# Kernel optimization log

Measured on AMD Instinct MI355X. Metric: run time of the kernel, lower is better.

Reference implementation:

```python
import jax, jax.numpy as jnp
import numpy as np

EPS = 1e-5  # torch BatchNorm default


def setup_inputs() -> dict:
    key = jax.random.key(0)
    ks = jax.random.split(key, 8)
    B, Q, S, C = 4, 256, 128, 256
    feats = [2 * C, 256, 64, 1]  # opt['num_features']
    inp = {
        "support_features": jax.random.normal(ks[0], (B, S, C), dtype=jnp.float32),
        "query_features": jax.random.normal(ks[1], (B, Q, C), dtype=jnp.float32),
    }
    for i in range(3):
        fan_in, fan_out = feats[i], feats[i + 1]
        std = np.sqrt(2.0 / (fan_in + fan_out))  # xavier_normal on conv weight
        inp[f"W{i}"] = jax.random.normal(ks[2 + i], (fan_out, fan_in), dtype=jnp.float32) * std
        inp[f"b{i}"] = jnp.zeros((fan_out,), dtype=jnp.float32)
        inp[f"g{i}"] = jnp.ones((fan_out,), dtype=jnp.float32)   # BN weight
        inp[f"bt{i}"] = jnp.zeros((fan_out,), dtype=jnp.float32)  # BN bias
    return inp


def _bn_relu(x, g, bt):
    # x: [B, N, C]; BatchNorm1d training-mode stats over batch and length dims
    mean = jnp.mean(x, axis=(0, 1))
    var = jnp.mean(jnp.square(x - mean), axis=(0, 1))  # biased var, as torch BN
    return jax.nn.relu((x - mean) * (g * jax.lax.rsqrt(var + EPS)) + bt)


def reference(support_features, query_features,
              W0, b0, g0, bt0, W1, b1, g1, bt1, W2, b2, g2, bt2):
    B, S, C = support_features.shape
    Q = query_features.shape[1]
    # pairwise concat: [B, Q, S, 2C]
    uq = jnp.broadcast_to(query_features[:, :, None, :], (B, Q, S, C))
    us = jnp.broadcast_to(support_features[:, None, :, :], (B, Q, S, C))
    x = jnp.concatenate([uq, us], axis=3).reshape(B, Q * S, 2 * C)
    # 1x1 conv == matmul over channel dim
    x = _bn_relu(jnp.einsum('bnc,oc->bno', x, W0) + b0, g0, bt0)
    x = _bn_relu(jnp.einsum('bnc,oc->bno', x, W1) + b1, g1, bt1)
    x = _bn_relu(jnp.einsum('bnc,oc->bno', x, W2) + b2, g2, bt2)
    # back to [B, C_out, Q, S]
    return jnp.transpose(x, (0, 2, 1)).reshape(B, -1, Q, S)
```

## Files before the change

### kernel.cpp

```cpp
#include <hip/hip_runtime.h>
#include <hip/hip_bf16.h>


typedef __attribute__((ext_vector_type(4))) float f32x4;
typedef __attribute__((ext_vector_type(8))) short s16x8;

#define BN_EPS 1e-5f
#define INV_N  (1.0f/131072.0f)

__device__ __forceinline__ unsigned pk_bf16(float a, float b) {
  float2 t; t.x = a; t.y = b;
  __hip_bfloat162 h = __float22bfloat162_rn(t);
  return *reinterpret_cast<unsigned*>(&h);
}
__device__ __forceinline__ void split2(float a, float b, unsigned& uh, unsigned& ul) {
  uh = pk_bf16(a, b);
  float ha = __uint_as_float(uh << 16);
  float hb = __uint_as_float(uh & 0xFFFF0000u);
  ul = pk_bf16(a - ha, b - hb);
}

union frag_u { s16x8 v; unsigned u[4]; };

struct Args {
  const float *Sf, *Qf, *W0, *b0, *g0, *bt0, *W1, *b1, *g1, *bt1, *W2, *b2, *g2, *bt2;
  float *Aq, *As, *y2, *ws0s, *ws1f, *ws2f, *out;
  ushort *y1f;
};

__global__ __launch_bounds__(64) void k_g0(Args a)
{
  int bi = blockIdx.x, t = threadIdx.x;
  if (bi == 384) {
    for (int i = t; i < 2048; i += 64) a.ws1f[i] = 0.0f;
    if (t < 32) a.ws2f[t] = 0.0f;
    return;
  }
  int l15 = t & 15, quad = t >> 4;
  int chunk = bi >> 2, ntile = bi & 3;
  bool isQ = (chunk < 64);
  const float* X; float* Out; int m0, koff;
  if (isQ) { m0 = chunk * 16; X = a.Qf; Out = a.Aq; koff = 0; }
  else     { m0 = (chunk - 64) * 16; X = a.Sf; Out = a.As; koff = 256; }
  int n0 = ntile * 64;

  f32x4 acc[4] = {};
#pragma unroll
  for (int ko = 0; ko < 256; ko += 32) {
    const float* row = X + (m0 + l15) * 256 + ko + quad * 8;
    f32x4 v0 = *(const f32x4*)(row);
    f32x4 v1 = *(const f32x4*)(row + 4);
    frag_u ah, al;
#pragma unroll
    for (int j = 0; j < 2; j++) {
      split2(v0[2 * j], v0[2 * j + 1], ah.u[j], al.u[j]);
      split2(v1[2 * j], v1[2 * j + 1], ah.u[2 + j], al.u[2 + j]);
    }
#pragma unroll
    for (int nt = 0; nt < 4; nt++) {
      const float* wrow = a.W0 + (n0 + nt * 16 + l15) * 512 + koff + ko + quad * 8;
      f32x4 w0v = *(const f32x4*)(wrow);
      f32x4 w1v = *(const f32x4*)(wrow + 4);
      frag_u bh, bl;
      split2(w0v[0], w0v[1], bh.u[0], bl.u[0]);
      split2(w0v[2], w0v[3], bh.u[1], bl.u[1]);
      split2(w1v[0], w1v[1], bh.u[2], bl.u[2]);
      split2(w1v[2], w1v[3], bh.u[3], bl.u[3]);
      acc[nt] = __builtin_amdgcn_mfma_f32_16x16x32_bf16(ah.v, bh.v, acc[nt], 0, 0, 0);
      acc[nt] = __builtin_amdgcn_mfma_f32_16x16x32_bf16(al.v, bh.v, acc[nt], 0, 0, 0);
      acc[nt] = __builtin_amdgcn_mfma_f32_16x16x32_bf16(ah.v, bl.v, acc[nt], 0, 0, 0);
    }
  }
#pragma unroll
  for (int nt = 0; nt < 4; nt++) {
    int o = n0 + nt * 16 + l15;
    float bias = isQ ? 0.0f : a.b0[o];
    float cs = 0, cs2 = 0;
#pragma unroll
    for (int r = 0; r < 4; r++) {
      float y = acc[nt][r] + bias;
      Out[(m0 + quad * 4 + r) * 256 + o] = y;
      cs += y; cs2 += y * y;
    }
    cs  += __shfl_xor(cs, 16);  cs  += __shfl_xor(cs, 32);
    cs2 += __shfl_xor(cs2, 16); cs2 += __shfl_xor(cs2, 32);
    if (quad == 0) {
      a.ws0s[chunk * 512 + o] = cs;
      a.ws0s[chunk * 512 + 256 + o] = cs2;
    }
  }
}

__device__ __forceinline__ void bn0_finalize(const Args& a, int t, float* sh_a0c0)
{
  int o = t;
  float sumY = 0, cross = 0, SQ2 = 0, SS2 = 0;
#pragma unroll
  for (int b = 0; b < 4; b++) {
    float sq1 = 0, sq2 = 0, ss1 = 0, ss2 = 0;
#pragma unroll
    for (int c = 0; c < 16; c++) {
      sq1 += a.ws0s[(b * 16 + c) * 512 + o];
      sq2 += a.ws0s[(b * 16 + c) * 512 + 256 + o];
    }
#pragma unroll
    for (int c = 0; c < 8; c++) {
      ss1 += a.ws0s[(64 + b * 8 + c) * 512 + o];
      ss2 += a.ws0s[(64 + b * 8 + c) * 512 + 256 + o];
    }
    SQ2 += sq2; SS2 += ss2;
    sumY += 128.0f * sq1 + 256.0f * ss1;
    cross += sq1 * ss1;
  }
  float mean = sumY * INV_N;
  float var = (128.0f * SQ2 + 256.0f * SS2 + 2.0f * cross) * INV_N - mean * mean;
  float aa = a.g0[o] * rsqrtf(var + BN_EPS);
  sh_a0c0[o] = aa;
  sh_a0c0[256 + o] = a.bt0[o] - mean * aa;
}

__global__ __launch_bounds__(256) void k_m1(Args a)
{
  int bi = blockIdx.x, t = threadIdx.x;
  int w = t >> 6, l = t & 63, l15 = l & 15, quad = l >> 4;
  __shared__ ushort w1f[2048 * 8];
  __shared__ float sh_a0c0[512];
  __shared__ float red[2][4][4][16];

#pragma unroll
  for (int i = 0; i < 8; i++) {
    int fr = i * 256 + t;
    int kk = fr >> 8, r = fr & 255, nt = r >> 6, ln = r & 63;
    const float* src = a.W1 + (nt * 16 + (ln & 15)) * 256 + kk * 32 + (ln >> 4) * 8;
    f32x4 v0 = *(const f32x4*)(src);
    f32x4 v1 = *(const f32x4*)(src + 4);
    frag_u z;
    z.u[0] = pk_bf16(v0[0], v0[1]); z.u[1] = pk_bf16(v0[2], v0[3]);
    z.u[2] = pk_bf16(v1[0], v1[1]); z.u[3] = pk_bf16(v1[2], v1[3]);
    *(s16x8*)(w1f + fr * 8) = z.v;
  }
  bn0_finalize(a, t, sh_a0c0);
  __syncthreads();

  int b_ = bi >> 7, rem = bi & 127, qt = rem >> 3, st = rem & 7;
  const float* asrow = a.As + ((b_ << 7) + st * 16 + l15) * 256;
  const float* aqrow[4];
#pragma unroll
  for (int mt = 0; mt < 4; mt++)
    aqrow[mt] = a.Aq + ((b_ << 8) + qt * 16 + w * 4 + mt) * 256;

  f32x4 acc[4][4] = {};
#pragma unroll
  for (int kk = 0; kk < 8; kk++) {
    int obase = kk * 32 + quad * 8;
    f32x4 a0v0 = *(const f32x4*)(sh_a0c0 + obase);
    f32x4 a0v1 = *(const f32x4*)(sh_a0c0 + obase + 4);
    f32x4 c0v0 = *(const f32x4*)(sh_a0c0 + 256 + obase);
    f32x4 c0v1 = *(const f32x4*)(sh_a0c0 + 256 + obase + 4);
    f32x4 as0 = *(const f32x4*)(asrow + obase);
    f32x4 as1 = *(const f32x4*)(asrow + obase + 4);

    s16x8 zh[4];
#pragma unroll
    for (int mt = 0; mt < 4; mt++) {
      f32x4 aq0 = *(const f32x4*)(aqrow[mt] + obase);
      f32x4 aq1 = *(const f32x4*)(aqrow[mt] + obase + 4);
      f32x4 z0 = (aq0 + as0) * a0v0 + c0v0;
      f32x4 z1 = (aq1 + as1) * a0v1 + c0v1;
      frag_u zz;
      zz.u[0] = pk_bf16(fmaxf(z0[0], 0.0f), fmaxf(z0[1], 0.0f));
      zz.u[1] = pk_bf16(fmaxf(z0[2], 0.0f), fmaxf(z0[3], 0.0f));
      zz.u[2] = pk_bf16(fmaxf(z1[0], 0.0f), fmaxf(z1[1], 0.0f));
      zz.u[3] = pk_bf16(fmaxf(z1[2], 0.0f), fmaxf(z1[3], 0.0f));
      zh[mt] = zz.v;
    }
#pragma unroll
    for (int nt = 0; nt < 4; nt++) {
      s16x8 bw = *(const s16x8*)(w1f + ((kk * 4 + nt) * 64 + l) * 8);
#pragma unroll
      for (int mt = 0; mt < 4; mt++)
        acc[mt][nt] = __builtin_amdgcn_mfma_f32_16x16x32_bf16(zh[mt], bw, acc[mt][nt], 0, 0, 0);
    }
  }

  float biasv[4];
#pragma unroll
  for (int nt = 0; nt < 4; nt++) biasv[nt] = a.b1[nt * 16 + l15];
  float s[4] = {0, 0, 0, 0}, s2[4] = {0, 0, 0, 0};
#pragma unroll
  for (int mt = 0; mt < 4; mt++) {
#pragma unroll
    for (int nt = 0; nt < 4; nt++) {
      float y0 = acc[mt][nt][0] + biasv[nt];
      float y1 = acc[mt][nt][1] + biasv[nt];
      float y2v = acc[mt][nt][2] + biasv[nt];
      float y3 = acc[mt][nt][3] + biasv[nt];
      unsigned u01 = pk_bf16(y0, y1), u23 = pk_bf16(y2v, y3);
      uint2 pk; pk.x = u01; pk.y = u23;
      int slot = (bi * 4 + w) * 16 + mt * 4 + nt;
      *(uint2*)(a.y1f + (size_t)(slot * 64 + l) * 4) = pk;
      float f0 = __uint_as_float(u01 << 16), f1 = __uint_as_float(u01 & 0xFFFF0000u);
      float f2 = __uint_as_float(u23 << 16), f3 = __uint_as_float(u23 & 0xFFFF0000u);
      s[nt]  += f0 + f1 + f2 + f3;
      s2[nt] += f0 * f0 + f1 * f1 + f2 * f2 + f3 * f3;
    }
  }
#pragma unroll
  for (int nt = 0; nt < 4; nt++) {
    float v = s[nt], v2 = s2[nt];
    v  += __shfl_xor(v, 16);  v  += __shfl_xor(v, 32);
    v2 += __shfl_xor(v2, 16); v2 += __shfl_xor(v2, 32);
    if (quad == 0) { red[0][w][nt][l15] = v; red[1][w][nt][l15] = v2; }
  }
  __syncthreads();
  if (t < 128) {
    int which = t >> 6, j = t & 63, nt = j >> 4, jl = j & 15;
    float v = red[which][0][nt][jl] + red[which][1][nt][jl] +
              red[which][2][nt][jl] + red[which][3][nt][jl];
    atomicAdd(&a.ws1f[(bi & 15) * 128 + t], v);
  }
}

__global__ __launch_bounds__(256) void k_p2(Args a)
{
  int p = blockIdx.x, t = threadIdx.x;
  int w = t >> 6, l = t & 63, l15 = l & 15, quad = l >> 4;
  __shared__ float sh_tot[128];
  __shared__ float sh_a1c1[128];
  __shared__ float rs[16], rs2[16];

  if (t < 128) {
    float accv = 0;
#pragma unroll
    for (int c = 0; c < 16; c++) accv += a.ws1f[c * 128 + t];
    sh_tot[t] = accv;
  }
  __syncthreads();
  if (t < 64) {
    float mean = sh_tot[t] * INV_N;
    float var = sh_tot[64 + t] * INV_N - mean * mean;
    float aa = a.g1[t] * rsqrtf(var + BN_EPS);
    sh_a1c1[t] = aa;
    sh_a1c1[64 + t] = a.bt1[t] - mean * aa;
  }
  __syncthreads();

  float a1v[4], c1v[4], w2v[4];
#pragma unroll
  for (int nt = 0; nt < 4; nt++) {
    int j = nt * 16 + l15;
    a1v[nt] = sh_a1c1[j]; c1v[nt] = sh_a1c1[64 + j]; w2v[nt] = a.W2[j];
  }
  float b2v = a.b2[0];
  float ls = 0, ls2 = 0;

#pragma unroll
  for (int task = 0; task < 2; task++) {
    int gw = (p * 4 + w) * 2 + task;
    int bi = gw >> 2, w1 = gw & 3;
    int b = bi >> 7, rem = bi & 127, qt = rem >> 3, st = rem & 7;
#pragma unroll
    for (int mt = 0; mt < 4; mt++) {
      float part[4] = {0, 0, 0, 0};
#pragma unroll
      for (int nt = 0; nt < 4; nt++) {
        int slot = (bi * 4 + w1) * 16 + mt * 4 + nt;
        uint2 v = *(const uint2*)(a.y1f + (size_t)(slot * 64 + l) * 4);
        float f0 = __uint_as_float(v.x << 16), f1 = __uint_as_float(v.x & 0xFFFF0000u);
        float f2 = __uint_as_float(v.y << 16), f3 = __uint_as_float(v.y & 0xFFFF0000u);
        part[0] += fmaxf(a1v[nt] * f0 + c1v[nt], 0.0f) * w2v[nt];
        part[1] += fmaxf(a1v[nt] * f1 + c1v[nt], 0.0f) * w2v[nt];
        part[2] += fmaxf(a1v[nt] * f2 + c1v[nt], 0.0f) * w2v[nt];
        part[3] += fmaxf(a1v[nt] * f3 + c1v[nt], 0.0f) * w2v[nt];
      }
#pragma unroll
      for (int r = 0; r < 4; r++) {
        float pv = part[r];
        pv += __shfl_xor(pv, 1); pv += __shfl_xor(pv, 2);
        pv += __shfl_xor(pv, 4); pv += __shfl_xor(pv, 8);
        part[r] = pv + b2v;
      }
      if (l15 == 0) {
        int q = qt * 16 + w1 * 4 + mt;
        int P = ((b * 256 + q) * 128) + st * 16 + quad * 4;
        f32x4 o;
#pragma unroll
        for (int r = 0; r < 4; r++) { o[r] = part[r]; ls += part[r]; ls2 += part[r] * part[r]; }
        *(f32x4*)(a.y2 + P) = o;
      }
    }
  }
  if (l15 == 0) { rs[t >> 4] = ls; rs2[t >> 4] = ls2; }
  __syncthreads();
  if (t == 0) {
    float sv = 0, sv2 = 0;
#pragma unroll
    for (int i = 0; i < 16; i++) { sv += rs[i]; sv2 += rs2[i]; }
    atomicAdd(&a.ws2f[(p & 15) * 2], sv);
    atomicAdd(&a.ws2f[(p & 15) * 2 + 1], sv2);
  }
}

__global__ __launch_bounds__(256) void k_out(Args a)
{
  int t = threadIdx.x;
  float s = 0, s2 = 0;
#pragma unroll
  for (int c = 0; c < 16; c++) { s += a.ws2f[c * 2]; s2 += a.ws2f[c * 2 + 1]; }
  float mean = s * INV_N;
  float var = s2 * INV_N - mean * mean;
  float aa = a.g2[0] * rsqrtf(var + BN_EPS);
  float cc = a.bt2[0] - mean * aa;
  int i = (blockIdx.x * 256 + t) * 4;
  f32x4 v = *(const f32x4*)(a.y2 + i);
  f32x4 o;
#pragma unroll
  for (int r = 0; r < 4; r++) o[r] = fmaxf(aa * v[r] + cc, 0.0f);
  *(f32x4*)(a.out + i) = o;
}

extern "C" void kernel_launch(void* const* d_in, const int* in_sizes, int n_in,
                              void* d_out, int out_size, void* d_ws, size_t ws_size,
                              hipStream_t stream)
{
  float* ws = (float*)d_ws;
  Args a;
  a.Sf  = (const float*)d_in[0];
  a.Qf  = (const float*)d_in[1];
  a.W0  = (const float*)d_in[2];
  a.b0  = (const float*)d_in[3];
  a.g0  = (const float*)d_in[4];
  a.bt0 = (const float*)d_in[5];
  a.W1  = (const float*)d_in[6];
  a.b1  = (const float*)d_in[7];
  a.g1  = (const float*)d_in[8];
  a.bt1 = (const float*)d_in[9];
  a.W2  = (const float*)d_in[10];
  a.b2  = (const float*)d_in[11];
  a.g2  = (const float*)d_in[12];
  a.bt2 = (const float*)d_in[13];

  a.Aq   = ws;
  a.As   = ws + 262144;
  a.y2   = ws + 393216;
  a.ws0s = ws + 524288;
  a.ws1f = ws + 573440;
  a.ws2f = ws + 575488;
  a.y1f  = (ushort*)(ws + 575552);
  a.out  = (float*)d_out;

  k_g0 <<<385, 64, 0, stream>>>(a);
  k_m1 <<<512, 256, 0, stream>>>(a);
  k_p2 <<<256, 256, 0, stream>>>(a);
  k_out<<<128, 256, 0, stream>>>(a);
}
```

Baseline: 130.5 us.

## Fuse final BatchNorm/ReLU into k_p2 via grid-wide atomic barrier

```diff
diff --git a/kernel.cpp b/kernel.cpp
--- a/kernel.cpp
+++ b/kernel.cpp
@@ -24,7 +24,8 @@
 
 struct Args {
   const float *Sf, *Qf, *W0, *b0, *g0, *bt0, *W1, *b1, *g1, *bt1, *W2, *b2, *g2, *bt2;
-  float *Aq, *As, *y2, *ws0s, *ws1f, *ws2f, *out;
+  float *Aq, *As, *ws0s, *ws1f, *ws2f, *out;
+  unsigned *cnt;
   ushort *y1f;
 };
 
@@ -34,6 +35,7 @@
   if (bi == 384) {
     for (int i = t; i < 2048; i += 64) a.ws1f[i] = 0.0f;
     if (t < 32) a.ws2f[t] = 0.0f;
+    if (t == 0) *a.cnt = 0u;
     return;
   }
   int l15 = t & 15, quad = t >> 4;
@@ -228,6 +230,7 @@
   __shared__ float sh_tot[128];
   __shared__ float sh_a1c1[128];
   __shared__ float rs[16], rs2[16];
+  __shared__ float sh_fin[2];
 
   if (t < 128) {
     float accv = 0;
@@ -253,12 +256,12 @@
   }
   float b2v = a.b2[0];
   float ls = 0, ls2 = 0;
+  float keep[2][4][4];
 
 #pragma unroll
   for (int task = 0; task < 2; task++) {
     int gw = (p * 4 + w) * 2 + task;
     int bi = gw >> 2, w1 = gw & 3;
-    int b = bi >> 7, rem = bi & 127, qt = rem >> 3, st = rem & 7;
 #pragma unroll
     for (int mt = 0; mt < 4; mt++) {
       float part[4] = {0, 0, 0, 0};
@@ -278,45 +281,56 @@
         float pv = part[r];
         pv += __shfl_xor(pv, 1); pv += __shfl_xor(pv, 2);
         pv += __shfl_xor(pv, 4); pv += __shfl_xor(pv, 8);
-        part[r] = pv + b2v;
+        float y = pv + b2v;
+        keep[task][mt][r] = y;
+        if (l15 == 0) { ls += y; ls2 += y * y; }
       }
+    }
+  }
+  if (l15 == 0) { rs[t >> 4] = ls; rs2[t >> 4] = ls2; }
+  __syncthreads();
+
+  if (t == 0) {
+    float sv = 0, sv2 = 0;
+#pragma unroll
+    for (int i = 0; i < 16; i++) { sv += rs[i]; sv2 += rs2[i]; }
+    atomicAdd(&a.ws2f[(p & 15) * 2], sv);
+    atomicAdd(&a.ws2f[(p & 15) * 2 + 1], sv2);
+    __hip_atomic_fetch_add(a.cnt, 1u, __ATOMIC_ACQ_REL, __HIP_MEMORY_SCOPE_AGENT);
+    while (__hip_atomic_load(a.cnt, __ATOMIC_ACQUIRE, __HIP_MEMORY_SCOPE_AGENT) < 256u)
+      __builtin_amdgcn_s_sleep(2);
+    float s = 0, s2 = 0;
+#pragma unroll
+    for (int c = 0; c < 16; c++) {
+      s  += __hip_atomic_load(&a.ws2f[c * 2],     __ATOMIC_RELAXED, __HIP_MEMORY_SCOPE_AGENT);
+      s2 += __hip_atomic_load(&a.ws2f[c * 2 + 1], __ATOMIC_RELAXED, __HIP_MEMORY_SCOPE_AGENT);
+    }
+    float mean = s * INV_N;
+    float var = s2 * INV_N - mean * mean;
+    float aa = a.g2[0] * rsqrtf(var + BN_EPS);
+    sh_fin[0] = aa;
+    sh_fin[1] = a.bt2[0] - mean * aa;
+  }
+  __syncthreads();
+  float aav = sh_fin[0], ccv = sh_fin[1];
+
+#pragma unroll
+  for (int task = 0; task < 2; task++) {
+    int gw = (p * 4 + w) * 2 + task;
+    int bi = gw >> 2, w1 = gw & 3;
+    int b = bi >> 7, rem = bi & 127, qt = rem >> 3, st = rem & 7;
+#pragma unroll
+    for (int mt = 0; mt < 4; mt++) {
       if (l15 == 0) {
         int q = qt * 16 + w1 * 4 + mt;
         int P = ((b * 256 + q) * 128) + st * 16 + quad * 4;
         f32x4 o;
 #pragma unroll
-        for (int r = 0; r < 4; r++) { o[r] = part[r]; ls += part[r]; ls2 += part[r] * part[r]; }
-        *(f32x4*)(a.y2 + P) = o;
+        for (int r = 0; r < 4; r++) o[r] = fmaxf(aav * keep[task][mt][r] + ccv, 0.0f);
+        *(f32x4*)(a.out + P) = o;
       }
     }
   }
-  if (l15 == 0) { rs[t >> 4] = ls; rs2[t >> 4] = ls2; }
-  __syncthreads();
-  if (t == 0) {
-    float sv = 0, sv2 = 0;
-#pragma unroll
-    for (int i = 0; i < 16; i++) { sv += rs[i]; sv2 += rs2[i]; }
-    atomicAdd(&a.ws2f[(p & 15) * 2], sv);
-    atomicAdd(&a.ws2f[(p & 15) * 2 + 1], sv2);
-  }
-}
-
-__global__ __launch_bounds__(256) void k_out(Args a)
-{
-  int t = threadIdx.x;
-  float s = 0, s2 = 0;
-#pragma unroll
-  for (int c = 0; c < 16; c++) { s += a.ws2f[c * 2]; s2 += a.ws2f[c * 2 + 1]; }
-  float mean = s * INV_N;
-  float var = s2 * INV_N - mean * mean;
-  float aa = a.g2[0] * rsqrtf(var + BN_EPS);
-  float cc = a.bt2[0] - mean * aa;
-  int i = (blockIdx.x * 256 + t) * 4;
-  f32x4 v = *(const f32x4*)(a.y2 + i);
-  f32x4 o;
-#pragma unroll
-  for (int r = 0; r < 4; r++) o[r] = fmaxf(aa * v[r] + cc, 0.0f);
-  *(f32x4*)(a.out + i) = o;
 }
 
 extern "C" void kernel_launch(void* const* d_in, const int* in_sizes, int n_in,
@@ -342,15 +356,14 @@
 
   a.Aq   = ws;
   a.As   = ws + 262144;
-  a.y2   = ws + 393216;
   a.ws0s = ws + 524288;
   a.ws1f = ws + 573440;
   a.ws2f = ws + 575488;
+  a.cnt  = (unsigned*)(ws + 575520);
   a.y1f  = (ushort*)(ws + 575552);
   a.out  = (float*)d_out;
 
   k_g0 <<<385, 64, 0, stream>>>(a);
   k_m1 <<<512, 256, 0, stream>>>(a);
   k_p2 <<<256, 256, 0, stream>>>(a);
-  k_out<<<128, 256, 0, stream>>>(a);
-}
+}
```

After: 139.3 us. +6.7%, slower.
